# Kernel tuning notes

Measured on AMD Instinct MI355X. Metric: run time of the kernel, lower is better.

Reference implementation:

```python
import jax, jax.numpy as jnp
import numpy as np

N = 50000      # nodes
E = 800000     # edges
IN = 256       # in_dim
H = 8          # heads
C = 32         # out_dim per head (H*C == IN so residual is identity)
NEG_SLOPE = 0.2
LN_EPS = 1e-5


def setup_inputs() -> dict:
    key = jax.random.key(0)
    ks = jax.random.split(key, 8)
    x = jax.random.normal(ks[0], (N, IN), dtype=jnp.float32)
    edge_index = jax.random.randint(ks[1], (2, E), 0, N, dtype=jnp.int64)
    # GATConv params
    W = jax.random.normal(ks[2], (IN, H * C), dtype=jnp.float32) / np.sqrt(IN)
    att_src = jax.random.normal(ks[3], (H, C), dtype=jnp.float32) / np.sqrt(C)
    att_dst = jax.random.normal(ks[4], (H, C), dtype=jnp.float32) / np.sqrt(C)
    bias = jnp.zeros((H * C,), dtype=jnp.float32)
    # LayerNorm params
    ln_scale = jnp.ones((H * C,), dtype=jnp.float32)
    ln_bias = jnp.zeros((H * C,), dtype=jnp.float32)
    return {"x": x, "edge_index": edge_index, "W": W, "att_src": att_src,
            "att_dst": att_dst, "bias": bias, "ln_scale": ln_scale, "ln_bias": ln_bias}


def _gat_block(x, edge_index, W, att_src, att_dst, bias, ln_scale, ln_bias):
    src, dst = edge_index[0], edge_index[1]
    # linear projection -> [N, H, C]
    h = (x @ W).reshape(N, H, C)
    # per-node attention logits [N, H]
    a_src = jnp.einsum('nhc,hc->nh', h, att_src)
    a_dst = jnp.einsum('nhc,hc->nh', h, att_dst)
    # per-edge logits with LeakyReLU [E, H]
    alpha = jax.nn.leaky_relu(a_src[src] + a_dst[dst], NEG_SLOPE)
    # segment softmax over incoming edges of each destination node
    amax = jax.ops.segment_max(alpha, dst, num_segments=N)          # [N, H]
    amax = jnp.where(jnp.isfinite(amax), amax, 0.0)                 # empty segments
    ex = jnp.exp(alpha - amax[dst])                                 # [E, H]
    denom = jax.ops.segment_sum(ex, dst, num_segments=N)           # [N, H]
    attn = ex / (denom[dst] + 1e-16)                                # [E, H]
    # weighted message aggregation -> [N, H, C]
    msg = h[src] * attn[:, :, None]
    out = jax.ops.segment_sum(msg, dst, num_segments=N)
    out = out.reshape(N, H * C) + bias
    # residual (identity since in_dim == heads*out_dim), ELU, LayerNorm
    out = out + x
    out = jax.nn.elu(out)
    mu = jnp.mean(out, axis=-1, keepdims=True)
    var = jnp.var(out, axis=-1, keepdims=True)
    return (out - mu) * jax.lax.rsqrt(var + LN_EPS) * ln_scale + ln_bias


def reference(x, edge_index, W, att_src, att_dst, bias, ln_scale, ln_bias):
    return _gat_block(x, edge_index, W, att_src, att_dst, bias, ln_scale, ln_bias)
```

## Files before the change

kernel.cpp:

```cpp
#include <hip/hip_runtime.h>
#include <hip/hip_bf16.h>
#include <cstdint>

#define NN 50000
#define NE 800000
#define DIM 256
#define NH 8
#define NB 196

typedef short v8s __attribute__((ext_vector_type(8)));
typedef float v4f __attribute__((ext_vector_type(4)));
typedef unsigned short u16x8 __attribute__((ext_vector_type(8)));

__device__ __forceinline__ float b2f(unsigned short u) {
    union { float f; uint32_t i; } c; c.i = ((uint32_t)u) << 16; return c.f;
}
__device__ __forceinline__ unsigned short f2b(float f) {
    union { float f; uint32_t i; } c; c.f = f;
    uint32_t lsb = (c.i >> 16) & 1u;
    return (unsigned short)((c.i + 0x7FFFu + lsb) >> 16);
}

__global__ __launch_bounds__(256) void deg_kernel(const int* __restrict__ e,
                                                  int* __restrict__ deg) {
    const int i = blockIdx.x * 256 + threadIdx.x;
    const int lane = threadIdx.x & 63;
    int probe = e[2 * lane + 1];
    unsigned long long nz = __ballot(probe != 0);
    bool is64 = (nz == 0ull);
    int d = is64 ? e[2 * (NE + i)] : e[NE + i];
    atomicAdd(&deg[d], 1);
}

__global__ __launch_bounds__(256) void cvtw_kernel(const float* __restrict__ W,
                                                   unsigned short* __restrict__ Wt) {
    int idx = blockIdx.x * 256 + threadIdx.x;
    int k = idx >> 8, n = idx & 255;
    Wt[n * DIM + k] = f2b(W[k * DIM + n]);
}

#define LDA3 72
__global__ __launch_bounds__(512) void gemm_kernel(
    const float* __restrict__ X, const unsigned short* __restrict__ Wt,
    const float* __restrict__ ASRC, const float* __restrict__ ADST,
    unsigned short* __restrict__ H, float* __restrict__ a_srcG,
    float* __restrict__ a_dstG) {
    __shared__ __align__(16) unsigned short As[128 * LDA3];
    __shared__ __align__(16) unsigned short Bs[256 * LDA3];
    const int t = threadIdx.x;
    const int wave = t >> 6, lane = t & 63;
    const int wr = wave >> 2, wc = wave & 3;
    const int fr = lane & 15, fq = lane >> 4;
    const int m0 = blockIdx.x * 128;

    v4f acc[4][4];
    #pragma unroll
    for (int mi = 0; mi < 4; ++mi)
        #pragma unroll
        for (int j = 0; j < 4; ++j) acc[mi][j] = (v4f){0.f, 0.f, 0.f, 0.f};

    #pragma unroll
    for (int kt = 0; kt < 256; kt += 64) {
        #pragma unroll
        for (int it = 0; it < 4; ++it) {
            int v = t + it * 512;
            int row = v >> 4;
            int c4 = (v & 15) << 2;
            int gr = m0 + row;
            float4 val = make_float4(0.f, 0.f, 0.f, 0.f);
            if (gr < NN) val = *(const float4*)(X + (size_t)gr * DIM + kt + c4);
            ushort4 o;
            o.x = f2b(val.x); o.y = f2b(val.y); o.z = f2b(val.z); o.w = f2b(val.w);
            *(ushort4*)(As + row * LDA3 + c4) = o;
        }
        #pragma unroll
        for (int it = 0; it < 4; ++it) {
            int v = t + it * 512;
            int row = v >> 3;
            int kv = (v & 7) << 3;
            u16x8 val = *(const u16x8*)(Wt + (size_t)row * DIM + kt + kv);
            *(u16x8*)(Bs + row * LDA3 + kv) = val;
        }
        __syncthreads();
        #pragma unroll
        for (int ks = 0; ks < 64; ks += 32) {
            v8s a[4];
            #pragma unroll
            for (int mi = 0; mi < 4; ++mi)
                a[mi] = *(const v8s*)(As + (wr * 64 + mi * 16 + fr) * LDA3 + ks + fq * 8);
            #pragma unroll
            for (int j = 0; j < 4; ++j) {
                v8s b = *(const v8s*)(Bs + (wc * 64 + j * 16 + fr) * LDA3 + ks + fq * 8);
                #pragma unroll
                for (int mi = 0; mi < 4; ++mi)
                    acc[mi][j] = __builtin_amdgcn_mfma_f32_16x16x32_bf16(a[mi], b, acc[mi][j], 0, 0, 0);
            }
        }
        __syncthreads();
    }

    float asv[4], adv[4];
    #pragma unroll
    for (int j = 0; j < 4; ++j) {
        int hidx = 2 * wc + (j >> 1);
        int cidx = ((j & 1) << 4) + fr;
        asv[j] = ASRC[hidx * 32 + cidx];
        adv[j] = ADST[hidx * 32 + cidx];
    }
    #pragma unroll
    for (int mi = 0; mi < 4; ++mi) {
        float tSA[4], tSB[4], tDA[4], tDB[4];
        #pragma unroll
        for (int r = 0; r < 4; ++r) {
            tSA[r] = acc[mi][0][r] * asv[0] + acc[mi][1][r] * asv[1];
            tSB[r] = acc[mi][2][r] * asv[2] + acc[mi][3][r] * asv[3];
            tDA[r] = acc[mi][0][r] * adv[0] + acc[mi][1][r] * adv[1];
            tDB[r] = acc[mi][2][r] * adv[2] + acc[mi][3][r] * adv[3];
            #pragma unroll
            for (int off = 1; off <= 8; off <<= 1) {
                tSA[r] += __shfl_xor(tSA[r], off);
                tSB[r] += __shfl_xor(tSB[r], off);
                tDA[r] += __shfl_xor(tDA[r], off);
                tDB[r] += __shfl_xor(tDB[r], off);
            }
        }
        if (fr == 0) {
            #pragma unroll
            for (int r = 0; r < 4; ++r) {
                int gr = m0 + wr * 64 + mi * 16 + fq * 4 + r;
                if (gr < NN) {
                    a_srcG[gr * NH + 2 * wc]     = tSA[r];
                    a_srcG[gr * NH + 2 * wc + 1] = tSB[r];
                    a_dstG[gr * NH + 2 * wc]     = tDA[r];
                    a_dstG[gr * NH + 2 * wc + 1] = tDB[r];
                }
            }
        }
    }

    #pragma unroll
    for (int mi = 0; mi < 4; ++mi)
        #pragma unroll
        for (int j = 0; j < 4; ++j)
            #pragma unroll
            for (int r = 0; r < 4; ++r) {
                int gr = m0 + wr * 64 + mi * 16 + fq * 4 + r;
                int gc = wc * 64 + j * 16 + fr;
                if (gr < NN) H[(size_t)gr * DIM + gc] = f2b(acc[mi][j][r]);
            }
}

__global__ __launch_bounds__(256) void scan1_kernel(const int* __restrict__ deg,
                                                    int* __restrict__ row_start,
                                                    int* __restrict__ bsum) {
    const int t = threadIdx.x, b = blockIdx.x;
    const int i = b * 256 + t;
    const int lane = t & 63, wave = t >> 6;
    int v = (i < NN) ? deg[i] : 0;
    int x = v;
    #pragma unroll
    for (int off = 1; off <= 32; off <<= 1) {
        int y = __shfl_up(x, off);
        if (lane >= off) x += y;
    }
    __shared__ int wt[4];
    if (lane == 63) wt[wave] = x;
    __syncthreads();
    int add = 0;
    #pragma unroll
    for (int w2 = 0; w2 < 4; ++w2) if (w2 < wave) add += wt[w2];
    int incl = x + add;
    if (i < NN) row_start[i] = incl - v;
    if (t == 255) bsum[b] = incl;
}

__global__ __launch_bounds__(256) void scan2_kernel(const int* __restrict__ bsum,
                                                    int* __restrict__ boff,
                                                    int* __restrict__ row_start) {
    const int t = threadIdx.x;
    const int lane = t & 63, wave = t >> 6;
    int v = (t < NB) ? bsum[t] : 0;
    int x = v;
    #pragma unroll
    for (int off = 1; off <= 32; off <<= 1) {
        int y = __shfl_up(x, off);
        if (lane >= off) x += y;
    }
    __shared__ int wt[4];
    if (lane == 63) wt[wave] = x;
    __syncthreads();
    int add = 0;
    #pragma unroll
    for (int w2 = 0; w2 < 4; ++w2) if (w2 < wave) add += wt[w2];
    int incl = x + add;
    if (t < NB) boff[t] = incl - v;
    if (t == 255) row_start[NN] = incl;
}

__global__ __launch_bounds__(256) void scan3_kernel(int* __restrict__ row_start,
                                                    const int* __restrict__ boff,
                                                    int* __restrict__ cursor) {
    const int i = blockIdx.x * 256 + threadIdx.x;
    if (i < NN) {
        int r = row_start[i] + boff[blockIdx.x];
        row_start[i] = r;
        cursor[i] = r;
    }
}

__global__ __launch_bounds__(256) void fill_kernel(
    const int* __restrict__ e, const float* __restrict__ a_src,
    const float* __restrict__ a_dst, int* __restrict__ cursor,
    int* __restrict__ csr_src, float* __restrict__ wcsr) {
    const int i = blockIdx.x * 256 + threadIdx.x;
    const int lane = threadIdx.x & 63;
    int probe = e[2 * lane + 1];
    unsigned long long nz = __ballot(probe != 0);
    bool is64 = (nz == 0ull);
    int s, d;
    if (is64) { s = e[2 * i]; d = e[2 * (NE + i)]; }
    else      { s = e[i];     d = e[NE + i]; }
    int pos = atomicAdd(&cursor[d], 1);
    csr_src[pos] = s;
    float4 as0 = *(const float4*)(a_src + (size_t)s * NH);
    float4 as1 = *(const float4*)(a_src + (size_t)s * NH + 4);
    float4 ad0 = *(const float4*)(a_dst + (size_t)d * NH);
    float4 ad1 = *(const float4*)(a_dst + (size_t)d * NH + 4);
    const float* asp0 = (const float*)&as0; const float* asp1 = (const float*)&as1;
    const float* adp0 = (const float*)&ad0; const float* adp1 = (const float*)&ad1;
    float4 w0, w1;
    float* wp0 = (float*)&w0; float* wp1 = (float*)&w1;
    #pragma unroll
    for (int h = 0; h < 4; ++h) {
        float lg = asp0[h] + adp0[h];
        lg = lg > 0.f ? lg : 0.2f * lg;
        wp0[h] = __expf(lg);
        float lg2 = asp1[h] + adp1[h];
        lg2 = lg2 > 0.f ? lg2 : 0.2f * lg2;
        wp1[h] = __expf(lg2);
    }
    *(float4*)(wcsr + (size_t)pos * NH) = w0;
    *(float4*)(wcsr + (size_t)pos * NH + 4) = w1;
}

__global__ __launch_bounds__(256) void agg_kernel(
    const unsigned short* __restrict__ H, const int* __restrict__ row_start,
    const int* __restrict__ csr_src, const float* __restrict__ wcsr,
    const float* __restrict__ X, const float* __restrict__ BIAS,
    const float* __restrict__ LNS, const float* __restrict__ LNB,
    float* __restrict__ OUT) {
    const int wave = threadIdx.x >> 6, lane = threadIdx.x & 63;
    const int d = blockIdx.x * 4 + wave;
    if (d >= NN) return;
    const int base = row_start[d];
    const int degree = row_start[d + 1] - base;
    const int slot = lane >> 5;
    const int q = lane & 31;
    const int headq = q >> 2;

    float4 x0 = *(const float4*)(X + (size_t)d * DIM + q * 8);
    float4 x1 = *(const float4*)(X + (size_t)d * DIM + q * 8 + 4);
    float4 b0 = *(const float4*)(BIAS + q * 8);
    float4 b1 = *(const float4*)(BIAS + q * 8 + 4);
    float4 sc0 = *(const float4*)(LNS + q * 8);
    float4 sc1 = *(const float4*)(LNS + q * 8 + 4);
    float4 lb0 = *(const float4*)(LNB + q * 8);
    float4 lb1 = *(const float4*)(LNB + q * 8 + 4);

    float acc[8];
    #pragma unroll
    for (int j = 0; j < 8; ++j) acc[j] = 0.f;
    float sumw = 0.f;

    for (int c0 = 0; c0 < degree; c0 += 8) {
        const int e0 = c0 + slot * 4;
        const int rem = degree - e0;
        const size_t eb = (size_t)base + e0;
        int s0 = 0, s1 = 0, s2 = 0, s3 = 0;
        float w0 = 0.f, w1 = 0.f, w2 = 0.f, w3 = 0.f;
        if (rem > 0) { s0 = csr_src[eb];     w0 = wcsr[eb * NH + headq]; }
        if (rem > 1) { s1 = csr_src[eb + 1]; w1 = wcsr[(eb + 1) * NH + headq]; }
        if (rem > 2) { s2 = csr_src[eb + 2]; w2 = wcsr[(eb + 2) * NH + headq]; }
        if (rem > 3) { s3 = csr_src[eb + 3]; w3 = wcsr[(eb + 3) * NH + headq]; }
        u16x8 hv0 = *(const u16x8*)(H + (size_t)s0 * DIM + q * 8);
        u16x8 hv1 = *(const u16x8*)(H + (size_t)s1 * DIM + q * 8);
        u16x8 hv2 = *(const u16x8*)(H + (size_t)s2 * DIM + q * 8);
        u16x8 hv3 = *(const u16x8*)(H + (size_t)s3 * DIM + q * 8);
        sumw += (w0 + w1) + (w2 + w3);
        #pragma unroll
        for (int j = 0; j < 8; ++j) acc[j] += w0 * b2f(hv0[j]);
        #pragma unroll
        for (int j = 0; j < 8; ++j) acc[j] += w1 * b2f(hv1[j]);
        #pragma unroll
        for (int j = 0; j < 8; ++j) acc[j] += w2 * b2f(hv2[j]);
        #pragma unroll
        for (int j = 0; j < 8; ++j) acc[j] += w3 * b2f(hv3[j]);
    }

    float sum_ex = sumw + __shfl_xor(sumw, 32);
    #pragma unroll
    for (int j = 0; j < 8; ++j) acc[j] += __shfl_xor(acc[j], 32);

    const float inv = 1.0f / (sum_ex + 1e-16f);

    const float* xp0 = (const float*)&x0; const float* xp1 = (const float*)&x1;
    const float* bp0 = (const float*)&b0; const float* bp1 = (const float*)&b1;
    float v[8];
    float s1v = 0.f, s2v = 0.f;
    #pragma unroll
    for (int j = 0; j < 8; ++j) {
        float xv = (j < 4) ? xp0[j] : xp1[j - 4];
        float bv = (j < 4) ? bp0[j] : bp1[j - 4];
        float t = acc[j] * inv + bv + xv;
        t = t > 0.f ? t : expm1f(t);
        v[j] = t;
        s1v += t;
        s2v += t * t;
    }
    #pragma unroll
    for (int off = 16; off >= 1; off >>= 1) {
        s1v += __shfl_xor(s1v, off);
        s2v += __shfl_xor(s2v, off);
    }
    const float mean = s1v * (1.0f / 256.0f);
    float var = s2v * (1.0f / 256.0f) - mean * mean;
    var = fmaxf(var, 0.f);
    const float rstd = rsqrtf(var + 1e-5f);

    if (slot == 0) {
        const float* scp0 = (const float*)&sc0; const float* scp1 = (const float*)&sc1;
        const float* lbp0 = (const float*)&lb0; const float* lbp1 = (const float*)&lb1;
        float4 o0, o1;
        float* op0 = (float*)&o0; float* op1 = (float*)&o1;
        #pragma unroll
        for (int j = 0; j < 4; ++j) {
            op0[j] = (v[j] - mean) * rstd * scp0[j] + lbp0[j];
            op1[j] = (v[j + 4] - mean) * rstd * scp1[j] + lbp1[j];
        }
        *(float4*)(OUT + (size_t)d * DIM + q * 8) = o0;
        *(float4*)(OUT + (size_t)d * DIM + q * 8 + 4) = o1;
    }
}

extern "C" void kernel_launch(void* const* d_in, const int* in_sizes, int n_in,
                              void* d_out, int out_size, void* d_ws, size_t ws_size,
                              hipStream_t stream) {
    const float* X    = (const float*)d_in[0];
    const int*   EIDX = (const int*)d_in[1];
    const float* W    = (const float*)d_in[2];
    const float* ASRC = (const float*)d_in[3];
    const float* ADST = (const float*)d_in[4];
    const float* BIAS = (const float*)d_in[5];
    const float* LNS  = (const float*)d_in[6];
    const float* LNB  = (const float*)d_in[7];
    float* OUT = (float*)d_out;

    char* ws = (char*)d_ws;
    unsigned short* H  = (unsigned short*)(ws);
    unsigned short* Wt = (unsigned short*)(ws + 25600000);
    float* a_srcW      = (float*)(ws + 25731072);
    float* a_dstW      = (float*)(ws + 27331072);
    int*   deg         = (int*)(ws + 28931072);
    int*   row_start   = (int*)(ws + 29131072);
    int*   cursor      = (int*)(ws + 29331088);
    int*   csr_src     = (int*)(ws + 29531088);
    float* wcsr        = (float*)(ws + 32731136);
    int*   bsum        = (int*)(ws + 58331136);
    int*   boff        = (int*)(ws + 58331920);

    hipMemsetAsync(deg, 0, NN * sizeof(int), stream);

    dim3 blk(256);
    deg_kernel<<<dim3(NE / 256), blk, 0, stream>>>(EIDX, deg);
    scan1_kernel<<<dim3(NB), blk, 0, stream>>>(deg, row_start, bsum);
    scan2_kernel<<<dim3(1), blk, 0, stream>>>(bsum, boff, row_start);
    scan3_kernel<<<dim3(NB), blk, 0, stream>>>(row_start, boff, cursor);
    cvtw_kernel<<<dim3(256), blk, 0, stream>>>(W, Wt);
    gemm_kernel<<<dim3(391), dim3(512), 0, stream>>>(X, Wt, ASRC, ADST, H, a_srcW, a_dstW);
    fill_kernel<<<dim3(NE / 256), blk, 0, stream>>>(EIDX, a_srcW, a_dstW, cursor, csr_src, wcsr);
    agg_kernel<<<dim3((NN + 3) / 4), blk, 0, stream>>>(
        H, row_start, csr_src, wcsr, X, BIAS, LNS, LNB, OUT);
}
```

Baseline: 336.6 us.

## Shrink GEMM tile to 64 rows, split attention logits into own kernel, widen gather

The GEMM now uses 64-row tiles with 256 threads, giving twice as many blocks, and no longer computes the attention logits in its epilogue. A new att_kernel reads the bf16 H back and computes a_src/a_dst with a wave per node. The aggregation loop gathers 8 neighbour rows per half-wave per iteration instead of 4, to keep more memory loads in flight. The cost is an extra kernel launch and an extra pass over H. The logits are also now computed from bf16-rounded H rather than the fp32 accumulators, which changes precision slightly.

```diff
diff --git a/kernel.cpp b/kernel.cpp
--- a/kernel.cpp
+++ b/kernel.cpp
@@ -40,18 +40,15 @@
 }
 
 #define LDA3 72
-__global__ __launch_bounds__(512) void gemm_kernel(
+__global__ __launch_bounds__(256) void gemm_kernel(
     const float* __restrict__ X, const unsigned short* __restrict__ Wt,
-    const float* __restrict__ ASRC, const float* __restrict__ ADST,
-    unsigned short* __restrict__ H, float* __restrict__ a_srcG,
-    float* __restrict__ a_dstG) {
-    __shared__ __align__(16) unsigned short As[128 * LDA3];
+    unsigned short* __restrict__ H) {
+    __shared__ __align__(16) unsigned short As[64 * LDA3];
     __shared__ __align__(16) unsigned short Bs[256 * LDA3];
     const int t = threadIdx.x;
-    const int wave = t >> 6, lane = t & 63;
-    const int wr = wave >> 2, wc = wave & 3;
+    const int wc = t >> 6, lane = t & 63;
     const int fr = lane & 15, fq = lane >> 4;
-    const int m0 = blockIdx.x * 128;
+    const int m0 = blockIdx.x * 64;
 
     v4f acc[4][4];
     #pragma unroll
@@ -63,7 +60,7 @@
     for (int kt = 0; kt < 256; kt += 64) {
         #pragma unroll
         for (int it = 0; it < 4; ++it) {
-            int v = t + it * 512;
+            int v = t + it * 256;
             int row = v >> 4;
             int c4 = (v & 15) << 2;
             int gr = m0 + row;
@@ -74,8 +71,8 @@
             *(ushort4*)(As + row * LDA3 + c4) = o;
         }
         #pragma unroll
-        for (int it = 0; it < 4; ++it) {
-            int v = t + it * 512;
+        for (int it = 0; it < 8; ++it) {
+            int v = t + it * 256;
             int row = v >> 3;
             int kv = (v & 7) << 3;
             u16x8 val = *(const u16x8*)(Wt + (size_t)row * DIM + kt + kv);
@@ -87,7 +84,7 @@
             v8s a[4];
             #pragma unroll
             for (int mi = 0; mi < 4; ++mi)
-                a[mi] = *(const v8s*)(As + (wr * 64 + mi * 16 + fr) * LDA3 + ks + fq * 8);
+                a[mi] = *(const v8s*)(As + (mi * 16 + fr) * LDA3 + ks + fq * 8);
             #pragma unroll
             for (int j = 0; j < 4; ++j) {
                 v8s b = *(const v8s*)(Bs + (wc * 64 + j * 16 + fr) * LDA3 + ks + fq * 8);
@@ -98,56 +95,41 @@
         }
         __syncthreads();
     }
-
-    float asv[4], adv[4];
-    #pragma unroll
-    for (int j = 0; j < 4; ++j) {
-        int hidx = 2 * wc + (j >> 1);
-        int cidx = ((j & 1) << 4) + fr;
-        asv[j] = ASRC[hidx * 32 + cidx];
-        adv[j] = ADST[hidx * 32 + cidx];
-    }
-    #pragma unroll
-    for (int mi = 0; mi < 4; ++mi) {
-        float tSA[4], tSB[4], tDA[4], tDB[4];
-        #pragma unroll
-        for (int r = 0; r < 4; ++r) {
-            tSA[r] = acc[mi][0][r] * asv[0] + acc[mi][1][r] * asv[1];
-            tSB[r] = acc[mi][2][r] * asv[2] + acc[mi][3][r] * asv[3];
-            tDA[r] = acc[mi][0][r] * adv[0] + acc[mi][1][r] * adv[1];
-            tDB[r] = acc[mi][2][r] * adv[2] + acc[mi][3][r] * adv[3];
-            #pragma unroll
-            for (int off = 1; off <= 8; off <<= 1) {
-                tSA[r] += __shfl_xor(tSA[r], off);
-                tSB[r] += __shfl_xor(tSB[r], off);
-                tDA[r] += __shfl_xor(tDA[r], off);
-                tDB[r] += __shfl_xor(tDB[r], off);
-            }
-        }
-        if (fr == 0) {
-            #pragma unroll
-            for (int r = 0; r < 4; ++r) {
-                int gr = m0 + wr * 64 + mi * 16 + fq * 4 + r;
-                if (gr < NN) {
-                    a_srcG[gr * NH + 2 * wc]     = tSA[r];
-                    a_srcG[gr * NH + 2 * wc + 1] = tSB[r];
-                    a_dstG[gr * NH + 2 * wc]     = tDA[r];
-                    a_dstG[gr * NH + 2 * wc + 1] = tDB[r];
-                }
-            }
-        }
-    }
-
     #pragma unroll
     for (int mi = 0; mi < 4; ++mi)
         #pragma unroll
         for (int j = 0; j < 4; ++j)
             #pragma unroll
             for (int r = 0; r < 4; ++r) {
-                int gr = m0 + wr * 64 + mi * 16 + fq * 4 + r;
+                int gr = m0 + mi * 16 + fq * 4 + r;
                 int gc = wc * 64 + j * 16 + fr;
                 if (gr < NN) H[(size_t)gr * DIM + gc] = f2b(acc[mi][j][r]);
             }
+}
+
+__global__ __launch_bounds__(256) void att_kernel(
+    const unsigned short* __restrict__ H, const float* __restrict__ ASRC,
+    const float* __restrict__ ADST, float* __restrict__ a_src,
+    float* __restrict__ a_dst) {
+    const int wave = threadIdx.x >> 6, lane = threadIdx.x & 63;
+    const int n = blockIdx.x * 4 + wave;
+    if (n >= NN) return;
+    float4 as4 = *(const float4*)(ASRC + lane * 4);
+    float4 ad4 = *(const float4*)(ADST + lane * 4);
+    ushort4 hv = *(const ushort4*)(H + (size_t)n * DIM + lane * 4);
+    const unsigned short* hvp = (const unsigned short*)&hv;
+    float h0 = b2f(hvp[0]), h1 = b2f(hvp[1]), h2 = b2f(hvp[2]), h3 = b2f(hvp[3]);
+    float ps = h0 * as4.x + h1 * as4.y + h2 * as4.z + h3 * as4.w;
+    float pd = h0 * ad4.x + h1 * ad4.y + h2 * ad4.z + h3 * ad4.w;
+    #pragma unroll
+    for (int off = 1; off <= 4; off <<= 1) {
+        ps += __shfl_xor(ps, off);
+        pd += __shfl_xor(pd, off);
+    }
+    if ((lane & 7) == 0) {
+        a_src[n * NH + (lane >> 3)] = ps;
+        a_dst[n * NH + (lane >> 3)] = pd;
+    }
 }
 
 __global__ __launch_bounds__(256) void scan1_kernel(const int* __restrict__ deg,
@@ -272,29 +254,26 @@
     for (int j = 0; j < 8; ++j) acc[j] = 0.f;
     float sumw = 0.f;
 
-    for (int c0 = 0; c0 < degree; c0 += 8) {
-        const int e0 = c0 + slot * 4;
+    for (int c0 = 0; c0 < degree; c0 += 16) {
+        const int e0 = c0 + slot * 8;
         const int rem = degree - e0;
         const size_t eb = (size_t)base + e0;
-        int s0 = 0, s1 = 0, s2 = 0, s3 = 0;
-        float w0 = 0.f, w1 = 0.f, w2 = 0.f, w3 = 0.f;
-        if (rem > 0) { s0 = csr_src[eb];     w0 = wcsr[eb * NH + headq]; }
-        if (rem > 1) { s1 = csr_src[eb + 1]; w1 = wcsr[(eb + 1) * NH + headq]; }
-        if (rem > 2) { s2 = csr_src[eb + 2]; w2 = wcsr[(eb + 2) * NH + headq]; }
-        if (rem > 3) { s3 = csr_src[eb + 3]; w3 = wcsr[(eb + 3) * NH + headq]; }
-        u16x8 hv0 = *(const u16x8*)(H + (size_t)s0 * DIM + q * 8);
-        u16x8 hv1 = *(const u16x8*)(H + (size_t)s1 * DIM + q * 8);
-        u16x8 hv2 = *(const u16x8*)(H + (size_t)s2 * DIM + q * 8);
-        u16x8 hv3 = *(const u16x8*)(H + (size_t)s3 * DIM + q * 8);
-        sumw += (w0 + w1) + (w2 + w3);
-        #pragma unroll
-        for (int j = 0; j < 8; ++j) acc[j] += w0 * b2f(hv0[j]);
-        #pragma unroll
-        for (int j = 0; j < 8; ++j) acc[j] += w1 * b2f(hv1[j]);
-        #pragma unroll
-        for (int j = 0; j < 8; ++j) acc[j] += w2 * b2f(hv2[j]);
-        #pragma unroll
-        for (int j = 0; j < 8; ++j) acc[j] += w3 * b2f(hv3[j]);
+        int s[8]; float w[8];
+        #pragma unroll
+        for (int k = 0; k < 8; ++k) { s[k] = 0; w[k] = 0.f; }
+        #pragma unroll
+        for (int k = 0; k < 8; ++k)
+            if (rem > k) { s[k] = csr_src[eb + k]; w[k] = wcsr[(eb + k) * NH + headq]; }
+        u16x8 hv[8];
+        #pragma unroll
+        for (int k = 0; k < 8; ++k)
+            hv[k] = *(const u16x8*)(H + (size_t)s[k] * DIM + q * 8);
+        #pragma unroll
+        for (int k = 0; k < 8; ++k) {
+            sumw += w[k];
+            #pragma unroll
+            for (int j = 0; j < 8; ++j) acc[j] += w[k] * b2f(hv[k][j]);
+        }
     }
 
     float sum_ex = sumw + __shfl_xor(sumw, 32);
@@ -376,7 +355,8 @@
     scan2_kernel<<<dim3(1), blk, 0, stream>>>(bsum, boff, row_start);
     scan3_kernel<<<dim3(NB), blk, 0, stream>>>(row_start, boff, cursor);
     cvtw_kernel<<<dim3(256), blk, 0, stream>>>(W, Wt);
-    gemm_kernel<<<dim3(391), dim3(512), 0, stream>>>(X, Wt, ASRC, ADST, H, a_srcW, a_dstW);
+    gemm_kernel<<<dim3(782), blk, 0, stream>>>(X, Wt, H);
+    att_kernel<<<dim3((NN + 3) / 4), blk, 0, stream>>>(H, ASRC, ADST, a_srcW, a_dstW);
     fill_kernel<<<dim3(NE / 256), blk, 0, stream>>>(EIDX, a_srcW, a_dstW, cursor, csr_src, wcsr);
     agg_kernel<<<dim3((NN + 3) / 4), blk, 0, stream>>>(
         H, row_start, csr_src, wcsr, X, BIAS, LNS, LNB, OUT);
```

New measurement: 308.4 us. -8.4%, faster.
